# Performance work log

Measured on AMD Instinct MI355X. Metric: run time of the kernel, lower is better.

## Reference

```python
import jax, jax.numpy as jnp
import numpy as np

# module config (matches init_kwargs)
SLICE_W, SLICE_H = 32, 32
STRIDE, WIDTH_INIT = 8, 8
EMBED_DIM = 512
B, H, W = 64, 32, 4096
PAD = (SLICE_W - WIDTH_INIT) // 2  # 12, width padding with constant value 1.0


def setup_inputs() -> dict:
    key = jax.random.key(0)
    k1, k2, k3, k4, k5 = jax.random.split(key, 5)
    u = lambda k, s: jax.random.uniform(k, s, jnp.float32, -0.08, 0.08)
    return {
        "images": jax.random.normal(k1, (B, 1, H, W), jnp.float32),
        "conv_w": u(k2, (1, 1, 3, 3)),          # Conv2d(1,1,3x3) weight (OIHW)
        "conv_b": u(k3, (1,)),
        "lin_w": u(k4, (SLICE_W * SLICE_H, EMBED_DIM)),  # bridge Linear, stored [in,out]
        "lin_b": u(k5, (EMBED_DIM,)),
    }


def reference(images, conv_w, conv_b, lin_w, lin_b):
    b = images.shape[0]
    # pad width with constant 1 (F.pad(..., 'constant', 1))
    padded = jnp.pad(images, ((0, 0), (0, 0), (0, 0), (PAD, PAD)), constant_values=1.0)
    # vectorized replacement of the python loop over stride positions
    starts = np.arange(0, W - 1, STRIDE)               # [S] static
    S = starts.shape[0]                                # 512
    idx = starts[:, None] + np.arange(SLICE_W)[None, :]  # [S, slice_w]
    sl = padded[:, :, :, idx]                          # [B,1,H,S,slice_w]
    sl = jnp.transpose(sl, (0, 3, 1, 2, 4))            # [B,S,1,H,slice_w]
    x = sl.reshape(b * S, 1, H, SLICE_W)               # pixels
    # embedder: Conv2d(1,1,k=3,pad=1) + ReLU
    y = jax.lax.conv_general_dilated(x, conv_w, (1, 1), ((1, 1), (1, 1)))
    y = jax.nn.relu(y + conv_b[None, :, None, None])
    # bridge: Linear(slice_w*slice_h -> embed_dim)
    flat = y.reshape(b * S, H * SLICE_W)
    out = flat @ lin_w + lin_b
    return out.reshape(b, S, EMBED_DIM)
```

## Files before the change

### kernel.cpp

```cpp
#include <hip/hip_runtime.h>
#include <cstdint>
#include <cstddef>

typedef unsigned short u16;
typedef unsigned int   u32;
typedef __attribute__((ext_vector_type(4))) float  f32x4;
typedef __attribute__((ext_vector_type(2))) float  f32x2;
typedef __attribute__((ext_vector_type(2))) u32    u32x2;
typedef __attribute__((ext_vector_type(8))) __bf16 bf16x8;

#define PSW   1056
#define ASTR  72
#define CFW   4128
#define LROW  4128

#define WS_BT  0u
#define WS_CF  1048576u
#define WS_AB  (1048576u + 16908288u)
#define WS_NEED (1048576u + 16908288u + 4194304u)

static __device__ __forceinline__ float b2f(u32 u) {
  union { u32 i; float f; } c; c.i = u << 16; return c.f;
}
static __device__ __forceinline__ u16 f2b(float f) {
  union { float f; u32 i; } c; c.f = f;
  return (u16)((c.i + 0x7FFFu + ((c.i >> 16) & 1u)) >> 16);
}

static __device__ __forceinline__ void gl_lds16(const void* g, void* l) {
  __builtin_amdgcn_global_load_lds(
      (__attribute__((address_space(1))) unsigned int*)(void*)g,
      (__attribute__((address_space(3))) unsigned int*)l, 16, 0, 0);
}
static __device__ __forceinline__ void gl_lds4(const void* g, void* l) {
  __builtin_amdgcn_global_load_lds(
      (__attribute__((address_space(1))) unsigned int*)(void*)g,
      (__attribute__((address_space(3))) unsigned int*)l, 4, 0, 0);
}

__global__ __launch_bounds__(256) void transpose_w(const float* __restrict__ lw,
                                                   u16* __restrict__ bt) {
  __shared__ u16 tile[64][65];
  const int t  = threadIdx.x;
  const int c  = t & 63, r0 = t >> 6;
  const int n0 = blockIdx.x * 64;
  const int k0 = blockIdx.y * 64;
#pragma unroll
  for (int rr = 0; rr < 16; ++rr) {
    const int r = r0 * 16 + rr;
    tile[r][c] = f2b(lw[(size_t)(k0 + r) * 512 + n0 + c]);
  }
  __syncthreads();
#pragma unroll
  for (int rr = 0; rr < 16; ++rr) {
    const int r = r0 * 16 + rr;
    bt[(size_t)(n0 + r) * 1024 + k0 + c] = tile[c][r];
  }
}

__global__ __launch_bounds__(256) void prep5(
    const float* __restrict__ img, const float* __restrict__ cw,
    const float* __restrict__ cb, u16* __restrict__ cf, u32* __restrict__ ab,
    const float* __restrict__ lw, u16* __restrict__ bt)
{
  __shared__ __align__(16) float R[3][LROW];
  const int t  = threadIdx.x;
  const int id = blockIdx.x;

  if (id >= 2048) {
    u16* tile = (u16*)&R[0][0];
    const int T  = id - 2048;
    const int n0 = (T & 7) << 6, k0 = (T >> 3) << 6;
    const int c = t & 63, r0 = t >> 6;
#pragma unroll
    for (int rr = 0; rr < 16; ++rr) {
      const int r = r0 * 16 + rr;
      tile[r * 65 + c] = f2b(lw[(size_t)(k0 + r) * 512 + n0 + c]);
    }
    __syncthreads();
#pragma unroll
    for (int rr = 0; rr < 16; ++rr) {
      const int r = r0 * 16 + rr;
      bt[(size_t)(n0 + r) * 1024 + k0 + c] = tile[c * 65 + r];
    }
    return;
  }

  const int wg = ((id & 7) << 8) + (id >> 3);
  const int bb = wg >> 5, hh = wg & 31;
  const float* imgb = img + (size_t)bb * 32 * 4096;
  const int w4id = t >> 6;

#pragma unroll
  for (int r = 0; r < 3; ++r) {
    float* Rr = &R[r][0];
    const int hr = hh - 1 + r;
    if (hr >= 0 && hr <= 31) {
      const float* src = imgb + (ptrdiff_t)hr * 4096;
#pragma unroll
      for (int p = 0; p < 4; ++p)
        gl_lds16(src + ((t + (p << 8)) << 2),
                 Rr + 16 + (w4id << 8) + (p << 10));
      if (t < 4)       Rr[t] = 0.0f;
      else if (t < 16) Rr[t] = 1.0f;
      else if (t < 28) Rr[4096 + t] = 1.0f;
      else if (t < 32) Rr[4096 + t] = 0.0f;
    } else {
#pragma unroll
      for (int p = 0; p < 4; ++p)
        *(f32x4*)(Rr + ((t + (p << 8)) << 2)) = (f32x4)0.0f;
      if (t < 8) *(f32x4*)(Rr + 4096 + (t << 2)) = (f32x4)0.0f;
    }
  }
  __syncthreads();

  float w9[9];
#pragma unroll
  for (int q = 0; q < 9; ++q) w9[q] = cw[q];
  const float bias = cb[0];
  u16* cfrow = cf + (size_t)(bb * 32 + hh) * CFW;
  if (t == 0) *(uint4*)(cfrow + 4120) = make_uint4(0u, 0u, 0u, 0u);

  const float* R0 = &R[0][0];
  const float* R1 = &R[1][0];
  const float* R2 = &R[2][0];

  auto CONV4 = [&](int c4) {
    const int w4 = c4 << 2;
    const f32x4 a0 = *(const f32x4*)(R0 + w4), b0 = *(const f32x4*)(R0 + w4 + 4);
    const float c0 = R0[w4 + 8];
    const f32x4 a1 = *(const f32x4*)(R1 + w4), b1 = *(const f32x4*)(R1 + w4 + 4);
    const float c1 = R1[w4 + 8];
    const f32x4 a2 = *(const f32x4*)(R2 + w4), b2 = *(const f32x4*)(R2 + w4 + 4);
    const float c2 = R2[w4 + 8];
    float o0 = bias, o1 = bias, o2 = bias, o3 = bias;
    o0 += w9[0] * a0.w + w9[1] * b0.x + w9[2] * b0.y;
    o1 += w9[0] * b0.x + w9[1] * b0.y + w9[2] * b0.z;
    o2 += w9[0] * b0.y + w9[1] * b0.z + w9[2] * b0.w;
    o3 += w9[0] * b0.z + w9[1] * b0.w + w9[2] * c0;
    o0 += w9[3] * a1.w + w9[4] * b1.x + w9[5] * b1.y;
    o1 += w9[3] * b1.x + w9[4] * b1.y + w9[5] * b1.z;
    o2 += w9[3] * b1.y + w9[4] * b1.z + w9[5] * b1.w;
    o3 += w9[3] * b1.z + w9[4] * b1.w + w9[5] * c1;
    o0 += w9[6] * a2.w + w9[7] * b2.x + w9[8] * b2.y;
    o1 += w9[6] * b2.x + w9[7] * b2.y + w9[8] * b2.z;
    o2 += w9[6] * b2.y + w9[7] * b2.z + w9[8] * b2.w;
    o3 += w9[6] * b2.z + w9[7] * b2.w + w9[8] * c2;
    u32x2 pk;
    pk.x = (u32)f2b(fmaxf(o0, 0.f)) | ((u32)f2b(fmaxf(o1, 0.f)) << 16);
    pk.y = (u32)f2b(fmaxf(o2, 0.f)) | ((u32)f2b(fmaxf(o3, 0.f)) << 16);
    *(u32x2*)(cfrow + (c4 << 2)) = pk;
  };

  for (int c4 = t; c4 < 1030; c4 += 256) CONV4(c4);

  u32* abrow = ab + (size_t)(bb * 32 + hh) * 512;
#pragma unroll
  for (int ss = 0; ss < 2; ++ss) {
    const int s  = t + (ss << 8);
    const int X0 = (s << 3) + 4;
    float o0 = bias, o1 = bias;
    o0 += w9[1] * R0[X0]      + w9[2] * R0[X0 + 1];
    o1 += w9[0] * R0[X0 + 30] + w9[1] * R0[X0 + 31];
    o0 += w9[4] * R1[X0]      + w9[5] * R1[X0 + 1];
    o1 += w9[3] * R1[X0 + 30] + w9[4] * R1[X0 + 31];
    o0 += w9[7] * R2[X0]      + w9[8] * R2[X0 + 1];
    o1 += w9[6] * R2[X0 + 30] + w9[7] * R2[X0 + 31];
    abrow[s] = (u32)f2b(fmaxf(o0, 0.f)) | ((u32)f2b(fmaxf(o1, 0.f)) << 16);
  }
}

__global__ __launch_bounds__(256) void gemm_k2(
    const u16* __restrict__ cf, const u32* __restrict__ ab,
    const u16* __restrict__ bt, const float* __restrict__ lb,
    float* __restrict__ out)
{
  __shared__ __align__(16) char sm[2176 + 512 + 16384];
  u16* Ps   = (u16*)sm;
  u32* Ab32 = (u32*)(sm + 2176);
  u16* Bs   = (u16*)(sm + 2688);
  float* Cs = (float*)sm;

  const int t  = threadIdx.x;
  const int orig = blockIdx.y * 4 + blockIdx.x;
  const int wg   = ((orig & 7) << 8) + (orig >> 3);
  const int nt = wg & 3, mt = wg >> 2;
  const int b  = mt >> 3, sg = mt & 7;
  const int n0 = nt << 7;
  const int w  = t >> 6, i = t & 63;
  const int wr = w >> 1, wc = w & 1;
  const int lq = i >> 4, lr = i & 15;

  const int cB = (i & 7) ^ ((i >> 3) & 7);
  const u16* btp = bt + (size_t)(n0 + (w << 5) + (i >> 3)) * 1024 + (cB << 3);
  u16* BsW = Bs + (w << 11);

  const int rP  = (t >= 68) ? 1 : 0;
  const int ccP = t - 68 * rP;
  const u16* cfp = cf + (size_t)(b * 32 + rP) * CFW + (sg << 9) + (ccP << 3);
  u16* PsW = (u16*)((char*)Ps + (w << 10));

  const u32* abp = ab + (size_t)(b * 32 + (t >> 6)) * 512 + (sg << 6) + (t & 63);
  u32* AbW = Ab32 + (w << 6);

  f32x4 acc[2][4];
#pragma unroll
  for (int a = 0; a < 2; ++a)
#pragma unroll
    for (int c = 0; c < 4; ++c) acc[a][c] = (f32x4)0.0f;

  for (int kk = 0; kk < 16; ++kk) {
    __syncthreads();
    gl_lds16(btp,              BsW);
    gl_lds16(btp +  8 * 1024,  BsW + 512);
    gl_lds16(btp + 16 * 1024,  BsW + 1024);
    gl_lds16(btp + 24 * 1024,  BsW + 1536);
    if (t < 136) gl_lds16(cfp, PsW);
    if (t < 128) gl_lds4(abp, AbW);
    btp += 64; cfp += 2 * CFW; abp += 1024;
    __syncthreads();

#pragma unroll
    for (int kc = 0; kc < 2; ++kc) {
      const int bswz = (((kc << 2) + lq) ^ (lr & 7)) << 3;
      bf16x8 af[2], bfv[4];
#pragma unroll
      for (int im = 0; im < 2; ++im) {
        const int ml = wr * 32 + im * 16 + lr;
        af[im] = __builtin_bit_cast(bf16x8,
            *(const uint4*)(Ps + kc * 544 + ((ml + lq) << 3)));
        const u32 a32 = Ab32[kc * 64 + ml];
        union { u16 u; __bf16 h; } lo, hi;
        lo.u = (u16)(a32 & 0xffffu); hi.u = (u16)(a32 >> 16);
        if (lq == 0) af[im][0] = lo.h;
        if (lq == 3) af[im][7] = hi.h;
      }
#pragma unroll
      for (int jn = 0; jn < 4; ++jn) {
        const int n = wc * 64 + jn * 16 + lr;
        bfv[jn] = __builtin_bit_cast(bf16x8, *(const uint4*)(Bs + (n << 6) + bswz));
      }
#pragma unroll
      for (int im = 0; im < 2; ++im)
#pragma unroll
        for (int jn = 0; jn < 4; ++jn)
          acc[im][jn] = __builtin_amdgcn_mfma_f32_16x16x32_bf16(
              af[im], bfv[jn], acc[im][jn], 0, 0, 0);
    }
  }

  float lbv[4];
#pragma unroll
  for (int jn = 0; jn < 4; ++jn) lbv[jn] = lb[n0 + wc * 64 + jn * 16 + lr];

  const int erow = t >> 3, ecol = (t & 7) << 4;
  const int grow_base = (mt << 6) + ((erow >> 4) * 32) + (erow & 15);

#pragma unroll
  for (int im = 0; im < 2; ++im) {
    __syncthreads();
#pragma unroll
    for (int jn = 0; jn < 4; ++jn) {
      const int cl = wc * 64 + jn * 16 + lr;
#pragma unroll
      for (int r = 0; r < 4; ++r)
        Cs[(wr * 16 + lq * 4 + r) * 132 + cl] = acc[im][jn][r] + lbv[jn];
    }
    __syncthreads();
    const size_t grow = (size_t)(grow_base + im * 16);
    float* orow = out + grow * 512 + n0 + ecol;
    const float* crow = Cs + erow * 132 + ecol;
#pragma unroll
    for (int p = 0; p < 4; ++p)
      *(f32x4*)(orow + p * 4) = *(const f32x4*)(crow + p * 4);
  }
}

__global__ __launch_bounds__(256) void fused_fallback(
    const float* __restrict__ img, const float* __restrict__ cw,
    const float* __restrict__ cb, const u16* __restrict__ bt,
    const float* __restrict__ lb, float* __restrict__ out)
{
  __shared__ __align__(16) u16 Ps[4 * PSW];
  __shared__ __align__(16) u16 As[128 * ASTR];
  __shared__ __align__(16) u16 Bs[128 * ASTR];
  const int t = threadIdx.x, nt = blockIdx.x, mt = blockIdx.y;
  const int b = mt >> 2, s0 = (mt & 3) << 7, X0 = s0 << 3, n0 = nt << 7;
  const float* imgb = img + (size_t)b * 32 * 4096;
  float cwf[9];
#pragma unroll
  for (int q = 0; q < 9; ++q) cwf[q] = cw[q];
  const float bias = cb[0];
  const int wv = t >> 6, l = t & 63;
  const int wr = wv >> 1, wc = wv & 1, lq = l >> 4, lr = l & 15;
  const int sl = t >> 1, hsel = t & 1;
  f32x4 acc[4][4];
#pragma unroll
  for (int a = 0; a < 4; ++a)
#pragma unroll
    for (int c = 0; c < 4; ++c) acc[a][c] = (f32x4)0.0f;
  for (int kk = 0; kk < 16; ++kk) {
    const int h0 = kk << 1;
    __syncthreads();
    uint4 bsv[4];
#pragma unroll
    for (int p = 0; p < 4; ++p) {
      const int idx8 = t + (p << 8);
      const int n = idx8 >> 3, k8 = idx8 & 7;
      bsv[p] = *(const uint4*)(bt + (size_t)(n0 + n) * 1024 + (kk << 6) + (k8 << 3));
    }
    for (int idx = t; idx < 4 * PSW; idx += 256) {
      const int r = idx / PSW, xi = idx - r * PSW;
      const int h = h0 - 1 + r, x = X0 - 1 + xi;
      u16 v = 0;
      if (h >= 0 && h < 32 && x >= 0 && x < 4120)
        v = (x < 12 || x >= 4108) ? (u16)0x3F80 : f2b(imgb[h * 4096 + (x - 12)]);
      Ps[idx] = v;
    }
    __syncthreads();
    {
      const int pbase = (sl << 3);
#pragma unroll
      for (int wb = 0; wb < 32; wb += 16) {
        float o[16];
#pragma unroll
        for (int j = 0; j < 16; ++j) o[j] = bias;
#pragma unroll
        for (int dr = 0; dr < 3; ++dr) {
          const u16* p = Ps + (hsel + dr) * PSW + pbase + wb;
          const uint4 va = *(const uint4*)p;
          const uint4 vb = *(const uint4*)(p + 8);
          const u32   vc = *(const u32*)(p + 16);
          float win[18];
          win[0] = b2f(va.x & 0xffffu); win[1] = b2f(va.x >> 16);
          win[2] = b2f(va.y & 0xffffu); win[3] = b2f(va.y >> 16);
          win[4] = b2f(va.z & 0xffffu); win[5] = b2f(va.z >> 16);
          win[6] = b2f(va.w & 0xffffu); win[7] = b2f(va.w >> 16);
          win[8] = b2f(vb.x & 0xffffu); win[9] = b2f(vb.x >> 16);
          win[10] = b2f(vb.y & 0xffffu); win[11] = b2f(vb.y >> 16);
          win[12] = b2f(vb.z & 0xffffu); win[13] = b2f(vb.z >> 16);
          win[14] = b2f(vb.w & 0xffffu); win[15] = b2f(vb.w >> 16);
          win[16] = b2f(vc & 0xffffu);   win[17] = b2f(vc >> 16);
          if (wb == 0) win[0] = 0.f; else win[17] = 0.f;
          const float w0 = cwf[dr * 3], w1 = cwf[dr * 3 + 1], w2 = cwf[dr * 3 + 2];
#pragma unroll
          for (int j = 0; j < 16; ++j)
            o[j] += w0 * win[j] + w1 * win[j + 1] + w2 * win[j + 2];
        }
        u32 pk[8];
#pragma unroll
        for (int q = 0; q < 8; ++q)
          pk[q] = (u32)f2b(fmaxf(o[2 * q], 0.f)) | ((u32)f2b(fmaxf(o[2 * q + 1], 0.f)) << 16);
        uint4* dst = (uint4*)(As + sl * ASTR + (hsel << 5) + wb);
        dst[0] = make_uint4(pk[0], pk[1], pk[2], pk[3]);
        dst[1] = make_uint4(pk[4], pk[5], pk[6], pk[7]);
      }
    }
#pragma unroll
    for (int p = 0; p < 4; ++p) {
      const int idx8 = t + (p << 8);
      const int n = idx8 >> 3, k8 = idx8 & 7;
      *(uint4*)(Bs + n * ASTR + (k8 << 3)) = bsv[p];
    }
    __syncthreads();
#pragma unroll
    for (int kc = 0; kc < 2; ++kc) {
      const int ko = (kc << 5) + (lq << 3);
      bf16x8 af[4], bfv[4];
#pragma unroll
      for (int im = 0; im < 4; ++im)
        af[im] = __builtin_bit_cast(bf16x8,
            *(const uint4*)(As + (wr * 64 + im * 16 + lr) * ASTR + ko));
#pragma unroll
      for (int jn = 0; jn < 4; ++jn)
        bfv[jn] = __builtin_bit_cast(bf16x8,
            *(const uint4*)(Bs + (wc * 64 + jn * 16 + lr) * ASTR + ko));
#pragma unroll
      for (int im = 0; im < 4; ++im)
#pragma unroll
        for (int jn = 0; jn < 4; ++jn)
          acc[im][jn] = __builtin_amdgcn_mfma_f32_16x16x32_bf16(
              af[im], bfv[jn], acc[im][jn], 0, 0, 0);
    }
  }
#pragma unroll
  for (int jn = 0; jn < 4; ++jn) {
    const int col = n0 + wc * 64 + jn * 16 + lr;
    const float lbv = lb[col];
#pragma unroll
    for (int im = 0; im < 4; ++im) {
      const int row0 = (mt << 7) + wr * 64 + im * 16 + (lq << 2);
#pragma unroll
      for (int r = 0; r < 4; ++r)
        out[(size_t)(row0 + r) * 512 + col] = acc[im][jn][r] + lbv;
    }
  }
}

extern "C" void kernel_launch(void* const* d_in, const int* in_sizes, int n_in,
                              void* d_out, int out_size, void* d_ws, size_t ws_size,
                              hipStream_t stream) {
  const float* img = (const float*)d_in[0];
  const float* cw  = (const float*)d_in[1];
  const float* cb  = (const float*)d_in[2];
  const float* lw  = (const float*)d_in[3];
  const float* lb  = (const float*)d_in[4];
  float* out = (float*)d_out;

  u16* btw = (u16*)((char*)d_ws + WS_BT);

  if (ws_size >= WS_NEED) {
    u16* cfp = (u16*)((char*)d_ws + WS_CF);
    u32* abp = (u32*)((char*)d_ws + WS_AB);
    prep5<<<dim3(2176), 256, 0, stream>>>(img, cw, cb, cfp, abp, lw, btw);
    gemm_k2<<<dim3(4, 512), 256, 0, stream>>>(cfp, abp, btw, lb, out);
  } else {
    transpose_w<<<dim3(8, 16), 256, 0, stream>>>(lw, btw);
    fused_fallback<<<dim3(4, 256), 256, 0, stream>>>(img, cw, cb, btw, lb, out);
  }
}
```

Before: 149.5 us.

## Double-buffer GEMM LDS stages and merge A-operand loads into one 16B load

The GEMM main loop now uses two LDS buffers, issuing the next K-tile's global-to-LDS loads before computing the current one, with explicit vmcnt waits and barriers in place of two full __syncthreads per iteration. The per-thread 4-byte ab loads are replaced by 16-byte loads spread across threads, so every thread issues exactly five 16B direct-to-LDS loads per stage. The goal is to hide global latency behind MFMA work and cut the number of load instructions. The cost is roughly double the LDS footprint, which may lower occupancy, and hand-written waitcnt logic that is fragile.

```diff
diff --git a/kernel.cpp b/kernel.cpp
--- a/kernel.cpp
+++ b/kernel.cpp
@@ -14,6 +14,8 @@
 #define CFW   4128
 #define LROW  4128
 
+#define BUF3  20096
+
 #define WS_BT  0u
 #define WS_CF  1048576u
 #define WS_AB  (1048576u + 16908288u)
@@ -31,11 +33,6 @@
   __builtin_amdgcn_global_load_lds(
       (__attribute__((address_space(1))) unsigned int*)(void*)g,
       (__attribute__((address_space(3))) unsigned int*)l, 16, 0, 0);
-}
-static __device__ __forceinline__ void gl_lds4(const void* g, void* l) {
-  __builtin_amdgcn_global_load_lds(
-      (__attribute__((address_space(1))) unsigned int*)(void*)g,
-      (__attribute__((address_space(3))) unsigned int*)l, 4, 0, 0);
 }
 
 __global__ __launch_bounds__(256) void transpose_w(const float* __restrict__ lw,
@@ -170,15 +167,12 @@
   }
 }
 
-__global__ __launch_bounds__(256) void gemm_k2(
+__global__ __launch_bounds__(256) void gemm_k3(
     const u16* __restrict__ cf, const u32* __restrict__ ab,
     const u16* __restrict__ bt, const float* __restrict__ lb,
     float* __restrict__ out)
 {
-  __shared__ __align__(16) char sm[2176 + 512 + 16384];
-  u16* Ps   = (u16*)sm;
-  u32* Ab32 = (u32*)(sm + 2176);
-  u16* Bs   = (u16*)(sm + 2688);
+  __shared__ __align__(16) char sm[2 * BUF3];
   float* Cs = (float*)sm;
 
   const int t  = threadIdx.x;
@@ -193,15 +187,23 @@
 
   const int cB = (i & 7) ^ ((i >> 3) & 7);
   const u16* btp = bt + (size_t)(n0 + (w << 5) + (i >> 3)) * 1024 + (cB << 3);
-  u16* BsW = Bs + (w << 11);
-
-  const int rP  = (t >= 68) ? 1 : 0;
-  const int ccP = t - 68 * rP;
-  const u16* cfp = cf + (size_t)(b * 32 + rP) * CFW + (sg << 9) + (ccP << 3);
-  u16* PsW = (u16*)((char*)Ps + (w << 10));
-
-  const u32* abp = ab + (size_t)(b * 32 + (t >> 6)) * 512 + (sg << 6) + (t & 63);
-  u32* AbW = Ab32 + (w << 6);
+
+  const int q5 = (w << 6) + i;
+  const char* p5; int step5;
+  if (q5 < 136) {
+    const int rP5 = (q5 >= 68) ? 1 : 0;
+    const int cc5 = q5 - 68 * rP5;
+    p5 = (const char*)(cf + (size_t)(b * 32 + rP5) * CFW + (sg << 9) + (cc5 << 3));
+    step5 = 2 * CFW * 2;
+  } else if (q5 < 168) {
+    const int a = q5 - 136;
+    p5 = (const char*)(ab + (size_t)(b * 32 + (a >> 4)) * 512 + (sg << 6) + ((a & 15) << 2));
+    step5 = 4096;
+  } else {
+    p5 = (const char*)btp;
+    step5 = 128;
+  }
+  const int off5 = (w == 3) ? 2688 : (w << 10);
 
   f32x4 acc[2][4];
 #pragma unroll
@@ -209,17 +211,20 @@
 #pragma unroll
     for (int c = 0; c < 4; ++c) acc[a][c] = (f32x4)0.0f;
 
-  for (int kk = 0; kk < 16; ++kk) {
-    __syncthreads();
+  auto STAGE = [&](char* base) {
+    u16* BsW = (u16*)(base + 3712) + (w << 11);
     gl_lds16(btp,              BsW);
     gl_lds16(btp +  8 * 1024,  BsW + 512);
     gl_lds16(btp + 16 * 1024,  BsW + 1024);
     gl_lds16(btp + 24 * 1024,  BsW + 1536);
-    if (t < 136) gl_lds16(cfp, PsW);
-    if (t < 128) gl_lds4(abp, AbW);
-    btp += 64; cfp += 2 * CFW; abp += 1024;
-    __syncthreads();
-
+    gl_lds16(p5, base + off5);
+    btp += 64; p5 += step5;
+  };
+
+  auto COMPUTE = [&](const char* base) {
+    const u16* Ps   = (const u16*)base;
+    const u32* Ab32 = (const u32*)(base + 2176);
+    const u16* Bs   = (const u16*)(base + 3712);
 #pragma unroll
     for (int kc = 0; kc < 2; ++kc) {
       const int bswz = (((kc << 2) + lq) ^ (lr & 7)) << 3;
@@ -247,7 +252,31 @@
           acc[im][jn] = __builtin_amdgcn_mfma_f32_16x16x32_bf16(
               af[im], bfv[jn], acc[im][jn], 0, 0, 0);
     }
-  }
+  };
+
+  char* bc = sm;
+  char* bn = sm + BUF3;
+  STAGE(bc);
+  asm volatile("s_waitcnt vmcnt(0)" ::: "memory");
+  __builtin_amdgcn_s_barrier();
+  asm volatile("" ::: "memory");
+
+#pragma unroll 1
+  for (int kk = 0; kk < 15; ++kk) {
+    STAGE(bn);
+    asm volatile("s_waitcnt vmcnt(5)" ::: "memory");
+    __builtin_amdgcn_s_barrier();
+    asm volatile("" ::: "memory");
+    COMPUTE(bc);
+    asm volatile("s_waitcnt lgkmcnt(0)" ::: "memory");
+    __builtin_amdgcn_s_barrier();
+    asm volatile("" ::: "memory");
+    char* tmp = bc; bc = bn; bn = tmp;
+  }
+  asm volatile("s_waitcnt vmcnt(0)" ::: "memory");
+  __builtin_amdgcn_s_barrier();
+  asm volatile("" ::: "memory");
+  COMPUTE(bc);
 
   float lbv[4];
 #pragma unroll
@@ -413,7 +442,7 @@
     u16* cfp = (u16*)((char*)d_ws + WS_CF);
     u32* abp = (u32*)((char*)d_ws + WS_AB);
     prep5<<<dim3(2176), 256, 0, stream>>>(img, cw, cb, cfp, abp, lw, btw);
-    gemm_k2<<<dim3(4, 512), 256, 0, stream>>>(cfp, abp, btw, lb, out);
+    gemm_k3<<<dim3(4, 512), 256, 0, stream>>>(cfp, abp, btw, lb, out);
   } else {
     transpose_w<<<dim3(8, 16), 256, 0, stream>>>(lw, btw);
     fused_fallback<<<dim3(4, 256), 256, 0, stream>>>(img, cw, cb, btw, lb, out);
```

Measured after the change: 152.0 us. No clear change (+1.7%).
